# Performance work log

Measured on AMD Instinct MI355X. Metric: run time of the kernel, lower is better.

## Reference

```python
import jax, jax.numpy as jnp
import numpy as np

N_USERS = 8000
N_ENTITIES = 32000
EMB = 64
N_HOPS = 2
N_GROUPS = 4
N_EDGES = 200000
TAU = 0.5


def _l2norm(x):
    # F.normalize(x, p=2, dim=1): x / max(||x||_2, eps)
    n = jnp.sqrt(jnp.sum(x * x, axis=1, keepdims=True))
    return x / jnp.maximum(n, 1e-12)


def setup_inputs() -> dict:
    key = jax.random.key(0)
    ks = jax.random.split(key, 8)
    return {
        "user_emb": jax.random.normal(ks[0], (N_USERS, EMB), jnp.float32),
        "user_ui_emb": jax.random.normal(ks[1], (N_USERS, EMB), jnp.float32),
        "entity_emb": jax.random.normal(ks[2], (N_ENTITIES, EMB), jnp.float32),
        "W1": jax.random.normal(ks[3], (EMB, EMB), jnp.float32) * 0.05,
        "b1": jnp.zeros((EMB,), jnp.float32),
        "W2": jax.random.normal(ks[4], (EMB, EMB), jnp.float32) * 0.05,
        "b2": jnp.zeros((EMB,), jnp.float32),
        "ui_index": jax.random.randint(ks[5], (N_GROUPS, N_EDGES), 0, N_USERS),
        "ei_index": jax.random.randint(ks[6], (N_GROUPS, N_EDGES), 0, N_ENTITIES),
        "mess_dropout": 0,  # eval mode: dropout disabled for deterministic reference
    }


def reference(user_emb, user_ui_emb, entity_emb, W1, b1, W2, b2,
              ui_index, ei_index, mess_dropout):
    accs = []    # per-group accumulated user embeddings
    scores = []  # per-group attention logits
    for g in range(N_GROUPS):
        ui = ui_index[g]  # [E] user index per edge
        ei = ei_index[g]  # [E] entity index per edge
        u_agg = user_emb
        e_int = entity_emb
        acc = jnp.zeros_like(user_emb)
        for _hop in range(N_HOPS):
            u_prev = u_agg
            u_msg = e_int[ei]   # gather entity->user messages per edge [E, D]
            e_msg = u_prev[ui]  # gather user->entity messages per edge [E, D]
            u_agg = jax.ops.segment_sum(u_msg, ui, num_segments=N_USERS)
            e_int = jax.ops.segment_sum(e_msg, ei, num_segments=N_ENTITIES)
            # mess_dropout == 0 in this reference (eval mode), so dropout is identity
            u_agg = _l2norm(u_agg)
            e_int = _l2norm(e_int)
            acc = acc + u_agg
        accs.append(acc)
        scores.append(jnp.sum(acc * user_ui_emb, axis=1))

    acc_stack = jnp.stack(accs, axis=1)                     # [U, G, D]
    att = jax.nn.softmax(jnp.stack(scores, axis=1), axis=1)  # [U, G]
    user_int_emb = jnp.sum(acc_stack * att[..., None], axis=1) + user_emb

    # Contrast_user: 2-layer ELU projection, cosine-sim InfoNCE at temperature tau
    def proj(z):
        return jax.nn.elu(z @ W1 + b1) @ W2 + b2

    p1 = _l2norm(proj(user_ui_emb))
    p2 = _l2norm(proj(user_int_emb))
    logits = (p1 @ p2.T) / TAU                              # [U, U]
    l12 = -jnp.diag(jax.nn.log_softmax(logits, axis=1))
    l21 = -jnp.diag(jax.nn.log_softmax(logits.T, axis=1))
    user_cl_loss = 0.5 * (jnp.mean(l12) + jnp.mean(l21))

    return (user_int_emb, user_cl_loss)
```

## Files before the change

kernel.cpp:

```cpp
#include <hip/hip_runtime.h>
#include <hip/hip_bf16.h>
#include <math.h>

#define N_USERS 8000
#define N_ENTITIES 32000
#define EMB 64
#define N_GROUPS 4
#define N_EDGES 200000

#define UBUCK 500
#define EBUCK 1000
#define UCAP 640
#define ECAP 384
#define BIN_CHUNK 2048
#define NRB 63

typedef __attribute__((ext_vector_type(8))) __bf16 bf16x8;
typedef __attribute__((ext_vector_type(16))) float f32x16;

static __device__ __forceinline__ unsigned short f2bf(float f) {
    union { float f; unsigned int i; } x; x.f = f;
    return (unsigned short)((x.i + 0x7FFF + ((x.i >> 16) & 1)) >> 16);
}
static __device__ __forceinline__ float u2f(unsigned int u) {
    union { unsigned int i; float f; } x; x.i = u; return x.f;
}

__global__ __launch_bounds__(256) void convert_tables(
    const float* __restrict__ ue, const float* __restrict__ ee,
    ushort* __restrict__ ueh, ushort* __restrict__ eeh)
{
    int i4 = blockIdx.x * 256 + threadIdx.x;
    if (i4 < 128000) {
        float4 v = ((const float4*)ue)[i4];
        ushort4 o; o.x = f2bf(v.x); o.y = f2bf(v.y); o.z = f2bf(v.z); o.w = f2bf(v.w);
        ((ushort4*)ueh)[i4] = o;
    } else if (i4 < 640000) {
        int j = i4 - 128000;
        float4 v = ((const float4*)ee)[j];
        ushort4 o; o.x = f2bf(v.x); o.y = f2bf(v.y); o.z = f2bf(v.z); o.w = f2bf(v.w);
        ((ushort4*)eeh)[j] = o;
    }
}

__global__ __launch_bounds__(256) void bin_edges(
    const int* __restrict__ ui_index, const int* __restrict__ ei_index,
    int* __restrict__ cnt_u, int* __restrict__ cnt_e,
    int* __restrict__ bin_u, int* __restrict__ bin_e)
{
    int g = blockIdx.y;
    const int* ui = ui_index + (size_t)g * N_EDGES;
    const int* ei = ei_index + (size_t)g * N_EDGES;
    __shared__ int hU[UBUCK], hE[EBUCK], bU[UBUCK], bE[EBUCK];
    int t = threadIdx.x;
    for (int i = t; i < UBUCK; i += 256) hU[i] = 0;
    for (int i = t; i < EBUCK; i += 256) hE[i] = 0;
    __syncthreads();
    int e0 = blockIdx.x * BIN_CHUNK;
    int us[8], vs[8];
    #pragma unroll
    for (int i = 0; i < 8; ++i) {
        int e = e0 + i * 256 + t;
        bool ok = e < N_EDGES;
        us[i] = ok ? ui[e] : -1;
        vs[i] = ok ? ei[e] : 0;
        if (ok) {
            atomicAdd(&hU[us[i] >> 4], 1);
            atomicAdd(&hE[vs[i] >> 5], 1);
        }
    }
    __syncthreads();
    for (int i = t; i < UBUCK; i += 256) {
        int c = hU[i];
        bU[i] = c ? atomicAdd(&cnt_u[g * UBUCK + i], c) : 0;
        hU[i] = 0;
    }
    for (int i = t; i < EBUCK; i += 256) {
        int c = hE[i];
        bE[i] = c ? atomicAdd(&cnt_e[g * EBUCK + i], c) : 0;
        hE[i] = 0;
    }
    __syncthreads();
    #pragma unroll
    for (int i = 0; i < 8; ++i) {
        if (us[i] >= 0) {
            int bu = us[i] >> 4;
            int s = atomicAdd(&hU[bu], 1) + bU[bu];
            if (s < UCAP)
                bin_u[((size_t)g * UBUCK + bu) * UCAP + s] = (us[i] & 15) | (vs[i] << 4);
            int be = vs[i] >> 5;
            int s2 = atomicAdd(&hE[be], 1) + bE[be];
            if (s2 < ECAP)
                bin_e[((size_t)g * EBUCK + be) * ECAP + s2] = (vs[i] & 31) | (us[i] << 5);
        }
    }
}

static __device__ __forceinline__ void map_gb(int gbase, int affin, int& g, int& b)
{
    if (affin) {
        int bid = blockIdx.x;
        int xcd = bid & 7;
        g = xcd >> 1;
        b = ((bid >> 3) << 1) | (xcd & 1);
    } else {
        g = gbase + blockIdx.y;
        b = blockIdx.x;
    }
}

__global__ __launch_bounds__(256) void agg_entity_b(
    const int* __restrict__ cnt_e, const int* __restrict__ bin_e,
    const ushort* __restrict__ ueh, ushort* __restrict__ ebufh,
    int gbase, int affin)
{
    int g, b;
    map_gb(gbase, affin, g, b);
    int gz = g - gbase;
    __shared__ int wds[ECAP];
    __shared__ int srt[ECAP];
    __shared__ int cnt[32];
    __shared__ int ptr[33];
    __shared__ int cur[32];
    int t = threadIdx.x;
    int count = min(cnt_e[g * EBUCK + b], ECAP);
    const int* bin = bin_e + ((size_t)g * EBUCK + b) * ECAP;
    if (t < 32) cnt[t] = 0;
    __syncthreads();
    for (int i = t; i < count; i += 256) {
        int w_ = bin[i];
        wds[i] = w_;
        atomicAdd(&cnt[w_ & 31], 1);
    }
    __syncthreads();
    if (t < 64) {
        int lane = t;
        int c = (lane < 32) ? cnt[lane] : 0;
        int val = c;
        #pragma unroll
        for (int off = 1; off < 32; off <<= 1) {
            int y = __shfl_up(val, off, 64);
            if (lane >= off) val += y;
        }
        if (lane < 32) {
            ptr[lane + 1] = val;
            cur[lane] = val - c;
            if (lane == 0) ptr[0] = 0;
        }
    }
    __syncthreads();
    for (int i = t; i < count; i += 256) {
        int w_ = wds[i];
        int pos = atomicAdd(&cur[w_ & 31], 1);
        srt[pos] = w_ >> 5;
    }
    __syncthreads();
    int wv = t >> 6, lane = t & 63, q = lane >> 4, d16 = lane & 15;
    for (int r = wv; r < 32; r += 4) {
        int start = ptr[r], end = ptr[r + 1];
        float a0 = 0.f, a1 = 0.f, a2 = 0.f, a3 = 0.f;
        for (int base = start; base < end; base += 8) {
            int i1 = base + q, i2 = base + 4 + q;
            int s1 = i1 < end ? srt[i1] : -1;
            int s2 = i2 < end ? srt[i2] : -1;
            unsigned x1 = s1 >= 0 ? (unsigned)s1 : 0u;
            unsigned x2 = s2 >= 0 ? (unsigned)s2 : 0u;
            uint2 r1 = *(const uint2*)(ueh + (x1 << 6) + (d16 << 2));
            uint2 r2 = *(const uint2*)(ueh + (x2 << 6) + (d16 << 2));
            if (s1 < 0) { r1.x = 0u; r1.y = 0u; }
            if (s2 < 0) { r2.x = 0u; r2.y = 0u; }
            a0 += u2f(r1.x << 16);
            a1 += u2f(r1.x & 0xFFFF0000u);
            a2 += u2f(r1.y << 16);
            a3 += u2f(r1.y & 0xFFFF0000u);
            a0 += u2f(r2.x << 16);
            a1 += u2f(r2.x & 0xFFFF0000u);
            a2 += u2f(r2.y << 16);
            a3 += u2f(r2.y & 0xFFFF0000u);
        }
        a0 += __shfl_xor(a0, 16); a0 += __shfl_xor(a0, 32);
        a1 += __shfl_xor(a1, 16); a1 += __shfl_xor(a1, 32);
        a2 += __shfl_xor(a2, 16); a2 += __shfl_xor(a2, 32);
        a3 += __shfl_xor(a3, 16); a3 += __shfl_xor(a3, 32);
        float ss = a0 * a0 + a1 * a1 + a2 * a2 + a3 * a3;
        #pragma unroll
        for (int off = 1; off < 16; off <<= 1) ss += __shfl_xor(ss, off);
        float inv = 1.0f / fmaxf(sqrtf(ss), 1e-12f);
        if (lane < 16) {
            ushort4 o;
            o.x = f2bf(a0 * inv); o.y = f2bf(a1 * inv);
            o.z = f2bf(a2 * inv); o.w = f2bf(a3 * inv);
            *(ushort4*)(ebufh + (size_t)gz * N_ENTITIES * EMB
                        + (((size_t)b * 32 + r) << 6) + (d16 << 2)) = o;
        }
    }
}

__global__ __launch_bounds__(256) void agg_user_b(
    const int* __restrict__ cnt_u, const int* __restrict__ bin_u,
    const ushort* __restrict__ eeh, const ushort* __restrict__ ebufh,
    float* __restrict__ acc, int gbase, int affin)
{
    int g, b;
    map_gb(gbase, affin, g, b);
    int gz = g - gbase;
    __shared__ int wds[UCAP];
    __shared__ int srt[UCAP];
    __shared__ int cnt[16];
    __shared__ int ptr[17];
    __shared__ int cur[16];
    int t = threadIdx.x;
    int count = min(cnt_u[g * UBUCK + b], UCAP);
    const int* bin = bin_u + ((size_t)g * UBUCK + b) * UCAP;
    const ushort* tabB = ebufh + (size_t)gz * N_ENTITIES * EMB;
    if (t < 16) cnt[t] = 0;
    __syncthreads();
    for (int i = t; i < count; i += 256) {
        int w_ = bin[i];
        wds[i] = w_;
        atomicAdd(&cnt[w_ & 15], 1);
    }
    __syncthreads();
    if (t < 64) {
        int lane = t;
        int c = (lane < 16) ? cnt[lane] : 0;
        int val = c;
        #pragma unroll
        for (int off = 1; off < 16; off <<= 1) {
            int y = __shfl_up(val, off, 64);
            if (lane >= off) val += y;
        }
        if (lane < 16) {
            ptr[lane + 1] = val;
            cur[lane] = val - c;
            if (lane == 0) ptr[0] = 0;
        }
    }
    __syncthreads();
    for (int i = t; i < count; i += 256) {
        int w_ = wds[i];
        int pos = atomicAdd(&cur[w_ & 15], 1);
        srt[pos] = w_ >> 4;
    }
    __syncthreads();
    int wv = t >> 6, lane = t & 63, q = lane >> 4, d16 = lane & 15;
    for (int r = wv; r < 16; r += 4) {
        int start = ptr[r], end = ptr[r + 1];
        float a0 = 0.f, a1 = 0.f, a2 = 0.f, a3 = 0.f;
        float b0 = 0.f, b1_ = 0.f, b2_ = 0.f, b3 = 0.f;
        for (int base = start; base < end; base += 8) {
            int i1 = base + q, i2 = base + 4 + q;
            int s1 = i1 < end ? srt[i1] : -1;
            int s2 = i2 < end ? srt[i2] : -1;
            unsigned o1 = ((s1 >= 0 ? (unsigned)s1 : 0u) << 6) + (d16 << 2);
            unsigned o2 = ((s2 >= 0 ? (unsigned)s2 : 0u) << 6) + (d16 << 2);
            uint2 ra1 = *(const uint2*)(eeh + o1);
            uint2 rb1 = *(const uint2*)(tabB + o1);
            uint2 ra2 = *(const uint2*)(eeh + o2);
            uint2 rb2 = *(const uint2*)(tabB + o2);
            if (s1 < 0) { ra1.x = 0u; ra1.y = 0u; rb1.x = 0u; rb1.y = 0u; }
            if (s2 < 0) { ra2.x = 0u; ra2.y = 0u; rb2.x = 0u; rb2.y = 0u; }
            a0 += u2f(ra1.x << 16) + u2f(ra2.x << 16);
            a1 += u2f(ra1.x & 0xFFFF0000u) + u2f(ra2.x & 0xFFFF0000u);
            a2 += u2f(ra1.y << 16) + u2f(ra2.y << 16);
            a3 += u2f(ra1.y & 0xFFFF0000u) + u2f(ra2.y & 0xFFFF0000u);
            b0  += u2f(rb1.x << 16) + u2f(rb2.x << 16);
            b1_ += u2f(rb1.x & 0xFFFF0000u) + u2f(rb2.x & 0xFFFF0000u);
            b2_ += u2f(rb1.y << 16) + u2f(rb2.y << 16);
            b3  += u2f(rb1.y & 0xFFFF0000u) + u2f(rb2.y & 0xFFFF0000u);
        }
        a0 += __shfl_xor(a0, 16); a0 += __shfl_xor(a0, 32);
        a1 += __shfl_xor(a1, 16); a1 += __shfl_xor(a1, 32);
        a2 += __shfl_xor(a2, 16); a2 += __shfl_xor(a2, 32);
        a3 += __shfl_xor(a3, 16); a3 += __shfl_xor(a3, 32);
        b0  += __shfl_xor(b0, 16);  b0  += __shfl_xor(b0, 32);
        b1_ += __shfl_xor(b1_, 16); b1_ += __shfl_xor(b1_, 32);
        b2_ += __shfl_xor(b2_, 16); b2_ += __shfl_xor(b2_, 32);
        b3  += __shfl_xor(b3, 16);  b3  += __shfl_xor(b3, 32);
        float ssA = a0 * a0 + a1 * a1 + a2 * a2 + a3 * a3;
        float ssB = b0 * b0 + b1_ * b1_ + b2_ * b2_ + b3 * b3;
        #pragma unroll
        for (int off = 1; off < 16; off <<= 1) {
            ssA += __shfl_xor(ssA, off);
            ssB += __shfl_xor(ssB, off);
        }
        float invA = 1.0f / fmaxf(sqrtf(ssA), 1e-12f);
        float invB = 1.0f / fmaxf(sqrtf(ssB), 1e-12f);
        if (lane < 16) {
            float4 o;
            o.x = a0 * invA + b0 * invB;
            o.y = a1 * invA + b1_ * invB;
            o.z = a2 * invA + b2_ * invB;
            o.w = a3 * invA + b3 * invB;
            *(float4*)(acc + (size_t)g * N_USERS * EMB
                       + (((size_t)b * 16 + r) << 6) + (d16 << 2)) = o;
        }
    }
}

__global__ __launch_bounds__(256) void combine_proj(
    const float* __restrict__ acc, const float* __restrict__ uie,
    const float* __restrict__ uemb,
    const float* __restrict__ W1, const float* __restrict__ b1,
    const float* __restrict__ W2, const float* __restrict__ b2,
    float* __restrict__ out_user,
    ushort* __restrict__ p1h, ushort* __restrict__ p2h,
    float* __restrict__ diag)
{
    __shared__ float W1s[EMB * EMB];
    __shared__ float W2s[EMB * EMB];
    __shared__ float zs[4][2][EMB];
    __shared__ float hs[4][2][EMB];
    int t = threadIdx.x;
    for (int i = t; i < EMB * EMB; i += 256) { W1s[i] = W1[i]; W2s[i] = W2[i]; }
    int w = t >> 6, lane = t & 63;
    int u = blockIdx.x * 4 + w;

    float ue = uie[(u << 6) + lane];
    float av[N_GROUPS], s[N_GROUPS];
    #pragma unroll
    for (int g = 0; g < N_GROUPS; ++g) {
        av[g] = acc[(size_t)g * N_USERS * EMB + (u << 6) + lane];
        float p = av[g] * ue;
        #pragma unroll
        for (int off = 1; off < 64; off <<= 1) p += __shfl_xor(p, off);
        s[g] = p;
    }
    float m = fmaxf(fmaxf(s[0], s[1]), fmaxf(s[2], s[3]));
    float att[N_GROUPS], tot = 0.f;
    #pragma unroll
    for (int g = 0; g < N_GROUPS; ++g) { att[g] = __expf(s[g] - m); tot += att[g]; }
    float inv = 1.0f / tot;
    float o = uemb[(u << 6) + lane];
    #pragma unroll
    for (int g = 0; g < N_GROUPS; ++g) o += att[g] * inv * av[g];
    out_user[(u << 6) + lane] = o;

    zs[w][0][lane] = ue;
    zs[w][1][lane] = o;
    __syncthreads();
    float h0 = b1[lane], h1 = b1[lane];
    #pragma unroll
    for (int k = 0; k < EMB; ++k) {
        float w1 = W1s[k * EMB + lane];
        h0 = fmaf(zs[w][0][k], w1, h0);
        h1 = fmaf(zs[w][1][k], w1, h1);
    }
    h0 = h0 > 0.f ? h0 : expm1f(h0);
    h1 = h1 > 0.f ? h1 : expm1f(h1);
    hs[w][0][lane] = h0;
    hs[w][1][lane] = h1;
    __syncthreads();
    float y0 = b2[lane], y1 = b2[lane];
    #pragma unroll
    for (int k = 0; k < EMB; ++k) {
        float w2 = W2s[k * EMB + lane];
        y0 = fmaf(hs[w][0][k], w2, y0);
        y1 = fmaf(hs[w][1][k], w2, y1);
    }
    float ss0 = y0 * y0, ss1 = y1 * y1;
    #pragma unroll
    for (int off = 1; off < 64; off <<= 1) {
        ss0 += __shfl_xor(ss0, off);
        ss1 += __shfl_xor(ss1, off);
    }
    float n0 = y0 / fmaxf(sqrtf(ss0), 1e-12f);
    float n1 = y1 / fmaxf(sqrtf(ss1), 1e-12f);
    p1h[(u << 6) + lane] = f2bf(n0);
    p2h[(u << 6) + lane] = f2bf(n1);
    float d = n0 * n1;
    #pragma unroll
    for (int off = 1; off < 64; off <<= 1) d += __shfl_xor(d, off);
    if (lane == 0) diag[u] = d * 2.0f;
}

#define NCHUNK 50
__global__ __launch_bounds__(256) void lse_tile(
    const ushort* __restrict__ Ah, const ushort* __restrict__ Bh,
    float* __restrict__ rowp, float* __restrict__ colp)
{
    __shared__ ushort Bs[160 * 68];
    __shared__ float cw[4][160];
    int t = threadIdx.x;
    int cb = blockIdx.x % 50;
    int rb = blockIdx.x / 50;
    int j0 = cb * 160;
    for (int slot = t; slot < 1280; slot += 256) {
        int row = slot >> 3;
        int o8 = (slot & 7) << 3;
        uint4 v = *(const uint4*)(Bh + (size_t)(j0 + row) * 64 + o8);
        ushort* dst = Bs + row * 68 + o8;
        *(uint2*)(dst + 0) = make_uint2(v.x, v.y);
        *(uint2*)(dst + 4) = make_uint2(v.z, v.w);
    }
    __syncthreads();
    int w = t >> 6, lane = t & 63;
    int strip = rb * 4 + w;
    bool alive = strip < 250;
    int i0 = alive ? strip * 32 : 0;
    int hl = lane >> 5, l31 = lane & 31;

    const bf16x8* A8 = (const bf16x8*)Ah;
    bf16x8 afrag[4];
    #pragma unroll
    for (int m = 0; m < 4; ++m)
        afrag[m] = A8[(i0 + l31) * 8 + m * 2 + hl];

    float rowacc[16];
    #pragma unroll
    for (int r = 0; r < 16; ++r) rowacc[r] = 0.f;

    #pragma unroll
    for (int cs = 0; cs < 5; ++cs) {
        bf16x8 bfrag[4];
        #pragma unroll
        for (int m = 0; m < 4; ++m) {
            const ushort* p = Bs + (cs * 32 + l31) * 68 + m * 16 + hl * 8;
            union { uint2 u[2]; bf16x8 f; } cv;
            cv.u[0] = *(const uint2*)p;
            cv.u[1] = *(const uint2*)(p + 4);
            bfrag[m] = cv.f;
        }
        f32x16 acc;
        #pragma unroll
        for (int r = 0; r < 16; ++r) acc[r] = 0.f;
        #pragma unroll
        for (int m = 0; m < 4; ++m)
            acc = __builtin_amdgcn_mfma_f32_32x32x16_bf16(afrag[m], bfrag[m], acc, 0, 0, 0);
        float e[16];
        #pragma unroll
        for (int r = 0; r < 16; ++r) {
            e[r] = __expf(acc[r] * 2.0f);
            rowacc[r] += e[r];
        }
        float c01 = (e[0] + e[1]) + (e[2] + e[3]);
        float c23 = (e[4] + e[5]) + (e[6] + e[7]);
        float c45 = (e[8] + e[9]) + (e[10] + e[11]);
        float c67 = (e[12] + e[13]) + (e[14] + e[15]);
        float csum = (c01 + c23) + (c45 + c67);
        csum += __shfl_xor(csum, 32);
        if (!alive) csum = 0.f;
        if (lane < 32) cw[w][cs * 32 + lane] = csum;
    }
    __syncthreads();
    if (t < 160)
        colp[rb * 8000 + j0 + t] = (cw[0][t] + cw[1][t]) + (cw[2][t] + cw[3][t]);
    if (alive) {
        #pragma unroll
        for (int r = 0; r < 16; ++r) {
            float v = rowacc[r];
            #pragma unroll
            for (int off = 1; off < 32; off <<= 1) v += __shfl_xor(v, off);
            if (l31 == 0)
                rowp[cb * 8000 + i0 + (r & 3) + 8 * (r >> 2) + 4 * hl] = v;
        }
    }
}

__global__ __launch_bounds__(256) void reduce_partials(
    const float* __restrict__ rowp, const float* __restrict__ colp,
    float* __restrict__ se_row, float* __restrict__ se_col)
{
    int id = blockIdx.x * 256 + threadIdx.x;
    if (id < N_USERS) {
        float s = 0.f;
        for (int c = 0; c < NCHUNK; ++c) s += rowp[c * 8000 + id];
        se_row[id] = s;
    } else if (id < 2 * N_USERS) {
        int j = id - N_USERS;
        float s = 0.f;
        for (int rb = 0; rb < NRB; ++rb) s += colp[rb * 8000 + j];
        se_col[j] = s;
    }
}

__global__ __launch_bounds__(256) void loss_kernel(
    const float* __restrict__ se_row, const float* __restrict__ se_col,
    const float* __restrict__ diag, float* __restrict__ out)
{
    __shared__ float red[256];
    int t = threadIdx.x;
    float s = 0.f;
    for (int i = t; i < N_USERS; i += 256)
        s += 0.5f * (logf(se_row[i]) + logf(se_col[i])) - diag[i];
    red[t] = s;
    __syncthreads();
    for (int w = 128; w > 0; w >>= 1) {
        if (t < w) red[t] += red[t + w];
        __syncthreads();
    }
    if (t == 0) out[0] = red[0] / (float)N_USERS;
}

extern "C" void kernel_launch(void* const* d_in, const int* in_sizes, int n_in,
                              void* d_out, int out_size, void* d_ws, size_t ws_size,
                              hipStream_t stream)
{
    const float* user_emb   = (const float*)d_in[0];
    const float* user_ui    = (const float*)d_in[1];
    const float* entity_emb = (const float*)d_in[2];
    const float* W1 = (const float*)d_in[3];
    const float* b1 = (const float*)d_in[4];
    const float* W2 = (const float*)d_in[5];
    const float* b2 = (const float*)d_in[6];
    const int* ui_index = (const int*)d_in[7];
    const int* ei_index = (const int*)d_in[8];

    float* ws = (float*)d_ws;
    float* acc    = ws;
    float* colp   = acc;
    float* se_row = ws + 2048000;
    float* se_col = se_row + 8000;
    float* diag   = se_col + 8000;
    ushort* p1h = (ushort*)(ws + 2072000);
    ushort* p2h = (ushort*)(ws + 2328000);
    float* rowp = ws + 2584000;
    int* cnt_u = (int*)(ws + 2984000);
    int* cnt_e = cnt_u + N_GROUPS * UBUCK;
    int* bin_u = cnt_e + N_GROUPS * EBUCK;
    int* bin_e = bin_u + N_GROUPS * UBUCK * UCAP;
    ushort* ueh = (ushort*)(ws + 5806000);
    ushort* eeh = (ushort*)(ws + 6062000);
    ushort* ebufh = (ushort*)(ws + 7086000);

    const size_t BASE_F = 7086000;
    int nG = 1;
    if (ws_size >= (BASE_F + 4 * 1024000) * 4) nG = 4;
    else if (ws_size >= (BASE_F + 2 * 1024000) * 4) nG = 2;

    float* out_user = (float*)d_out;
    float* out_loss = out_user + 512000;

    dim3 b256(256);

    hipMemsetAsync(cnt_u, 0, (size_t)N_GROUPS * (UBUCK + EBUCK) * 4, stream);
    convert_tables<<<2500, b256, 0, stream>>>(user_emb, entity_emb, ueh, eeh);
    bin_edges<<<dim3((N_EDGES + BIN_CHUNK - 1) / BIN_CHUNK, N_GROUPS), b256, 0, stream>>>(
        ui_index, ei_index, cnt_u, cnt_e, bin_u, bin_e);

    if (nG == 4) {
        agg_entity_b<<<EBUCK * 4, b256, 0, stream>>>(
            cnt_e, bin_e, ueh, ebufh, 0, 1);
        agg_user_b<<<UBUCK * 4, b256, 0, stream>>>(
            cnt_u, bin_u, eeh, ebufh, acc, 0, 1);
    } else {
        for (int gbase = 0; gbase < N_GROUPS; gbase += nG) {
            agg_entity_b<<<dim3(EBUCK, nG), b256, 0, stream>>>(
                cnt_e, bin_e, ueh, ebufh, gbase, 0);
            agg_user_b<<<dim3(UBUCK, nG), b256, 0, stream>>>(
                cnt_u, bin_u, eeh, ebufh, acc, gbase, 0);
        }
    }

    combine_proj<<<N_USERS / 4, b256, 0, stream>>>(
        acc, user_ui, user_emb, W1, b1, W2, b2,
        out_user, p1h, p2h, diag);

    lse_tile<<<NRB * 50, b256, 0, stream>>>(p1h, p2h, rowp, colp);
    reduce_partials<<<(2 * N_USERS + 255) / 256, b256, 0, stream>>>(
        rowp, colp, se_row, se_col);
    loss_kernel<<<1, b256, 0, stream>>>(se_row, se_col, diag, out_loss);
}
```

Measured before the change: 163.4 us.

## Fold memset and final reductions into kernels; unroll user gather loop by 16

Moves the zeroing of the bin counters into the convert kernel, dropping a separate memset launch. Merges the partial-sum reduction and the single-block loss kernel into one multi-block kernel that accumulates the loss with an atomic add, after zeroing it in combine_proj. Also widens the user aggregation gather loop to four rows per lane group per iteration for more memory-level parallelism. The atomic makes the float sum order nondeterministic, and the wider loop uses more registers.

```diff
diff --git a/kernel.cpp b/kernel.cpp
--- a/kernel.cpp
+++ b/kernel.cpp
@@ -14,6 +14,7 @@
 #define ECAP 384
 #define BIN_CHUNK 2048
 #define NRB 63
+#define NCHUNK 50
 
 typedef __attribute__((ext_vector_type(8))) __bf16 bf16x8;
 typedef __attribute__((ext_vector_type(16))) float f32x16;
@@ -28,8 +29,13 @@
 
 __global__ __launch_bounds__(256) void convert_tables(
     const float* __restrict__ ue, const float* __restrict__ ee,
-    ushort* __restrict__ ueh, ushort* __restrict__ eeh)
-{
+    ushort* __restrict__ ueh, ushort* __restrict__ eeh,
+    int* __restrict__ cnt)
+{
+    if (blockIdx.x == 0) {
+        for (int i = threadIdx.x; i < N_GROUPS * (UBUCK + EBUCK); i += 256)
+            cnt[i] = 0;
+    }
     int i4 = blockIdx.x * 256 + threadIdx.x;
     if (i4 < 128000) {
         float4 v = ((const float4*)ue)[i4];
@@ -248,26 +254,43 @@
         int start = ptr[r], end = ptr[r + 1];
         float a0 = 0.f, a1 = 0.f, a2 = 0.f, a3 = 0.f;
         float b0 = 0.f, b1_ = 0.f, b2_ = 0.f, b3 = 0.f;
-        for (int base = start; base < end; base += 8) {
-            int i1 = base + q, i2 = base + 4 + q;
-            int s1 = i1 < end ? srt[i1] : -1;
-            int s2 = i2 < end ? srt[i2] : -1;
-            unsigned o1 = ((s1 >= 0 ? (unsigned)s1 : 0u) << 6) + (d16 << 2);
-            unsigned o2 = ((s2 >= 0 ? (unsigned)s2 : 0u) << 6) + (d16 << 2);
+        for (int base = start; base < end; base += 16) {
+            int s0_ = (base + q)      < end ? srt[base + q]      : -1;
+            int s1_ = (base + 4 + q)  < end ? srt[base + 4 + q]  : -1;
+            int s2_ = (base + 8 + q)  < end ? srt[base + 8 + q]  : -1;
+            int s3_ = (base + 12 + q) < end ? srt[base + 12 + q] : -1;
+            unsigned o0 = ((s0_ >= 0 ? (unsigned)s0_ : 0u) << 6) + (d16 << 2);
+            unsigned o1 = ((s1_ >= 0 ? (unsigned)s1_ : 0u) << 6) + (d16 << 2);
+            unsigned o2 = ((s2_ >= 0 ? (unsigned)s2_ : 0u) << 6) + (d16 << 2);
+            unsigned o3 = ((s3_ >= 0 ? (unsigned)s3_ : 0u) << 6) + (d16 << 2);
+            uint2 ra0 = *(const uint2*)(eeh + o0);
+            uint2 rb0 = *(const uint2*)(tabB + o0);
             uint2 ra1 = *(const uint2*)(eeh + o1);
             uint2 rb1 = *(const uint2*)(tabB + o1);
             uint2 ra2 = *(const uint2*)(eeh + o2);
             uint2 rb2 = *(const uint2*)(tabB + o2);
-            if (s1 < 0) { ra1.x = 0u; ra1.y = 0u; rb1.x = 0u; rb1.y = 0u; }
-            if (s2 < 0) { ra2.x = 0u; ra2.y = 0u; rb2.x = 0u; rb2.y = 0u; }
-            a0 += u2f(ra1.x << 16) + u2f(ra2.x << 16);
-            a1 += u2f(ra1.x & 0xFFFF0000u) + u2f(ra2.x & 0xFFFF0000u);
-            a2 += u2f(ra1.y << 16) + u2f(ra2.y << 16);
-            a3 += u2f(ra1.y & 0xFFFF0000u) + u2f(ra2.y & 0xFFFF0000u);
-            b0  += u2f(rb1.x << 16) + u2f(rb2.x << 16);
-            b1_ += u2f(rb1.x & 0xFFFF0000u) + u2f(rb2.x & 0xFFFF0000u);
-            b2_ += u2f(rb1.y << 16) + u2f(rb2.y << 16);
-            b3  += u2f(rb1.y & 0xFFFF0000u) + u2f(rb2.y & 0xFFFF0000u);
+            uint2 ra3 = *(const uint2*)(eeh + o3);
+            uint2 rb3 = *(const uint2*)(tabB + o3);
+            if (s0_ < 0) { ra0.x = ra0.y = rb0.x = rb0.y = 0u; }
+            if (s1_ < 0) { ra1.x = ra1.y = rb1.x = rb1.y = 0u; }
+            if (s2_ < 0) { ra2.x = ra2.y = rb2.x = rb2.y = 0u; }
+            if (s3_ < 0) { ra3.x = ra3.y = rb3.x = rb3.y = 0u; }
+            a0 += (u2f(ra0.x << 16) + u2f(ra1.x << 16))
+                + (u2f(ra2.x << 16) + u2f(ra3.x << 16));
+            a1 += (u2f(ra0.x & 0xFFFF0000u) + u2f(ra1.x & 0xFFFF0000u))
+                + (u2f(ra2.x & 0xFFFF0000u) + u2f(ra3.x & 0xFFFF0000u));
+            a2 += (u2f(ra0.y << 16) + u2f(ra1.y << 16))
+                + (u2f(ra2.y << 16) + u2f(ra3.y << 16));
+            a3 += (u2f(ra0.y & 0xFFFF0000u) + u2f(ra1.y & 0xFFFF0000u))
+                + (u2f(ra2.y & 0xFFFF0000u) + u2f(ra3.y & 0xFFFF0000u));
+            b0  += (u2f(rb0.x << 16) + u2f(rb1.x << 16))
+                 + (u2f(rb2.x << 16) + u2f(rb3.x << 16));
+            b1_ += (u2f(rb0.x & 0xFFFF0000u) + u2f(rb1.x & 0xFFFF0000u))
+                 + (u2f(rb2.x & 0xFFFF0000u) + u2f(rb3.x & 0xFFFF0000u));
+            b2_ += (u2f(rb0.y << 16) + u2f(rb1.y << 16))
+                 + (u2f(rb2.y << 16) + u2f(rb3.y << 16));
+            b3  += (u2f(rb0.y & 0xFFFF0000u) + u2f(rb1.y & 0xFFFF0000u))
+                 + (u2f(rb2.y & 0xFFFF0000u) + u2f(rb3.y & 0xFFFF0000u));
         }
         a0 += __shfl_xor(a0, 16); a0 += __shfl_xor(a0, 32);
         a1 += __shfl_xor(a1, 16); a1 += __shfl_xor(a1, 32);
@@ -305,13 +328,14 @@
     const float* __restrict__ W2, const float* __restrict__ b2,
     float* __restrict__ out_user,
     ushort* __restrict__ p1h, ushort* __restrict__ p2h,
-    float* __restrict__ diag)
+    float* __restrict__ diag, float* __restrict__ out_loss)
 {
     __shared__ float W1s[EMB * EMB];
     __shared__ float W2s[EMB * EMB];
     __shared__ float zs[4][2][EMB];
     __shared__ float hs[4][2][EMB];
     int t = threadIdx.x;
+    if (blockIdx.x == 0 && t == 0) out_loss[0] = 0.f;
     for (int i = t; i < EMB * EMB; i += 256) { W1s[i] = W1[i]; W2s[i] = W2[i]; }
     int w = t >> 6, lane = t & 63;
     int u = blockIdx.x * 4 + w;
@@ -374,7 +398,6 @@
     if (lane == 0) diag[u] = d * 2.0f;
 }
 
-#define NCHUNK 50
 __global__ __launch_bounds__(256) void lse_tile(
     const ushort* __restrict__ Ah, const ushort* __restrict__ Bh,
     float* __restrict__ rowp, float* __restrict__ colp)
@@ -457,39 +480,27 @@
     }
 }
 
-__global__ __launch_bounds__(256) void reduce_partials(
+__global__ __launch_bounds__(256) void finish_loss(
     const float* __restrict__ rowp, const float* __restrict__ colp,
-    float* __restrict__ se_row, float* __restrict__ se_col)
-{
-    int id = blockIdx.x * 256 + threadIdx.x;
+    const float* __restrict__ diag, float* __restrict__ out_loss)
+{
+    int t = threadIdx.x;
+    int id = blockIdx.x * 256 + t;
+    float s = 0.f;
     if (id < N_USERS) {
-        float s = 0.f;
-        for (int c = 0; c < NCHUNK; ++c) s += rowp[c * 8000 + id];
-        se_row[id] = s;
-    } else if (id < 2 * N_USERS) {
-        int j = id - N_USERS;
-        float s = 0.f;
-        for (int rb = 0; rb < NRB; ++rb) s += colp[rb * 8000 + j];
-        se_col[j] = s;
-    }
-}
-
-__global__ __launch_bounds__(256) void loss_kernel(
-    const float* __restrict__ se_row, const float* __restrict__ se_col,
-    const float* __restrict__ diag, float* __restrict__ out)
-{
+        float sr = 0.f, sc = 0.f;
+        for (int c = 0; c < NCHUNK; ++c) sr += rowp[c * 8000 + id];
+        for (int rb = 0; rb < NRB; ++rb) sc += colp[rb * 8000 + id];
+        s = 0.5f * (logf(sr) + logf(sc)) - diag[id];
+    }
     __shared__ float red[256];
-    int t = threadIdx.x;
-    float s = 0.f;
-    for (int i = t; i < N_USERS; i += 256)
-        s += 0.5f * (logf(se_row[i]) + logf(se_col[i])) - diag[i];
     red[t] = s;
     __syncthreads();
     for (int w = 128; w > 0; w >>= 1) {
         if (t < w) red[t] += red[t + w];
         __syncthreads();
     }
-    if (t == 0) out[0] = red[0] / (float)N_USERS;
+    if (t == 0) atomicAdd(out_loss, red[0] * (1.0f / (float)N_USERS));
 }
 
 extern "C" void kernel_launch(void* const* d_in, const int* in_sizes, int n_in,
@@ -509,9 +520,7 @@
     float* ws = (float*)d_ws;
     float* acc    = ws;
     float* colp   = acc;
-    float* se_row = ws + 2048000;
-    float* se_col = se_row + 8000;
-    float* diag   = se_col + 8000;
+    float* diag   = ws + 2048000;
     ushort* p1h = (ushort*)(ws + 2072000);
     ushort* p2h = (ushort*)(ws + 2328000);
     float* rowp = ws + 2584000;
@@ -533,8 +542,7 @@
 
     dim3 b256(256);
 
-    hipMemsetAsync(cnt_u, 0, (size_t)N_GROUPS * (UBUCK + EBUCK) * 4, stream);
-    convert_tables<<<2500, b256, 0, stream>>>(user_emb, entity_emb, ueh, eeh);
+    convert_tables<<<2500, b256, 0, stream>>>(user_emb, entity_emb, ueh, eeh, cnt_u);
     bin_edges<<<dim3((N_EDGES + BIN_CHUNK - 1) / BIN_CHUNK, N_GROUPS), b256, 0, stream>>>(
         ui_index, ei_index, cnt_u, cnt_e, bin_u, bin_e);
 
@@ -554,10 +562,9 @@
 
     combine_proj<<<N_USERS / 4, b256, 0, stream>>>(
         acc, user_ui, user_emb, W1, b1, W2, b2,
-        out_user, p1h, p2h, diag);
+        out_user, p1h, p2h, diag, out_loss);
 
     lse_tile<<<NRB * 50, b256, 0, stream>>>(p1h, p2h, rowp, colp);
-    reduce_partials<<<(2 * N_USERS + 255) / 256, b256, 0, stream>>>(
-        rowp, colp, se_row, se_col);
-    loss_kernel<<<1, b256, 0, stream>>>(se_row, se_col, diag, out_loss);
-}
+    finish_loss<<<(N_USERS + 255) / 256, b256, 0, stream>>>(
+        rowp, colp, diag, out_loss);
+}
```

After: 152.4 us, median of 2. 1.07x faster.
